# Kernel optimization log

Measured on AMD Instinct MI355X. Metric: run time of the kernel, lower is better.

The kernel has to match this reference:

```python
import jax, jax.numpy as jnp
import numpy as np

EPS = 1e-05
MARGIN = 0.0


def setup_inputs() -> dict:
    key = jax.random.key(0)
    k1, k2 = jax.random.split(key)
    embeddings = jax.random.normal(k1, (512, 512), dtype=jnp.float32)
    labels = jax.random.randint(k2, (512,), 0, 32, dtype=jnp.int64)
    return {"embeddings": embeddings, "labels": labels}


def _pairwise_distance(e, squared=False):
    # e: [B, D] -> [B, B] euclidean distances
    dot = jnp.matmul(e, e.T)
    sq = jnp.diag(dot)
    d = sq[:, None] - 2.0 * dot + sq[None, :]
    d = jnp.maximum(d, 0.0)
    if not squared:
        zmask = (d == 0.0).astype(d.dtype)
        d = d + zmask * EPS
        d = jnp.sqrt(d) + EPS
        d = d * (1.0 - zmask)
    return d


def _triplet_mask(labels):
    B = labels.shape[0]
    not_eq = ~jnp.eye(B, dtype=bool)
    # distinct indices i != j, i != k, j != k  -> [B, B, B]
    distinct = not_eq[:, :, None] & not_eq[:, None, :] & not_eq[None, :, :]
    lab_eq = labels[None, :] == labels[:, None]  # symmetric [B, B]
    valid = lab_eq[:, :, None] & (~lab_eq[:, None, :])  # label[i]==label[j], label[i]!=label[k]
    return (distinct & valid).astype(jnp.float32)


def reference(embeddings, labels):
    d = _pairwise_distance(embeddings, squared=False)  # [B, B]
    # triplet_loss[a, p, n] = d[a, p] - d[a, n] + margin
    tl = d[:, :, None] - d[:, None, :] + MARGIN
    mask = _triplet_mask(labels)
    tl = jnp.maximum(mask * tl, 0.0)
    num_positive = jnp.sum((tl > 1e-05).astype(jnp.float32))
    num_valid = jnp.sum(mask)
    fraction_positive = num_positive / (num_valid + 1e-05)
    loss = jnp.sum(tl) / (num_positive + 1e-05)
    return (loss, fraction_positive)
```

## Files before the change

### kernel.cpp

```cpp
#include <hip/hip_runtime.h>

#define BSZ 512
#define EPSF 1e-5f
#define KT   32
#define NS   16
#define TR   128
#define TC   64
#define ASTR 132
#define BSTR 68

#define WS_PARTIAL 8
#define WS_P       2048

__device__ __forceinline__ float dist_xform(float v) {
    v = fmaxf(v, 0.0f);
    float z = (v == 0.0f) ? 1.0f : 0.0f;
    v = sqrtf(v + z * EPSF) + EPSF;
    return v * (1.0f - z);
}

__global__ __launch_bounds__(256) void dsq_kernel(const float* __restrict__ E,
                                                  float* __restrict__ ws) {
    if (blockIdx.x == 0 && blockIdx.y == 0 && blockIdx.z == 0 && threadIdx.x == 0) {
        ((int*)ws)[3] = 0;
    }

    __shared__ __align__(16) float As[KT][ASTR];
    __shared__ __align__(16) float Bs[KT][BSTR];
    const int tid = threadIdx.x;
    const int tx = tid & 15;
    const int ty = tid >> 4;
    const int bi = blockIdx.x * TR;
    const int bj = blockIdx.y * TC;
    const int k0 = blockIdx.z * KT;

    {
        const int r0 = tid >> 3;
        const int kc = (tid & 7) * 4;
#pragma unroll
        for (int p = 0; p < 4; ++p) {
            const int row = p * 32 + r0;
            float4 v = *(const float4*)(E + (size_t)(bi + row) * BSZ + k0 + kc);
            As[kc  ][row] = v.x; As[kc+1][row] = v.y; As[kc+2][row] = v.z; As[kc+3][row] = v.w;
        }
#pragma unroll
        for (int p = 0; p < 2; ++p) {
            const int row = p * 32 + r0;
            float4 v = *(const float4*)(E + (size_t)(bj + row) * BSZ + k0 + kc);
            Bs[kc  ][row] = v.x; Bs[kc+1][row] = v.y; Bs[kc+2][row] = v.z; Bs[kc+3][row] = v.w;
        }
    }
    __syncthreads();

    float acc[8][4];
#pragma unroll
    for (int r = 0; r < 8; ++r)
#pragma unroll
        for (int c = 0; c < 4; ++c) acc[r][c] = 0.0f;

#pragma unroll 4
    for (int kk = 0; kk < KT; ++kk) {
        float4 A0 = *(const float4*)&As[kk][ty * 8];
        float4 A1 = *(const float4*)&As[kk][ty * 8 + 4];
        float4 B0 = *(const float4*)&Bs[kk][tx * 4];
        float ar[8] = {A0.x, A0.y, A0.z, A0.w, A1.x, A1.y, A1.z, A1.w};
        float br[4] = {B0.x, B0.y, B0.z, B0.w};
#pragma unroll
        for (int r = 0; r < 8; ++r)
#pragma unroll
            for (int c = 0; c < 4; ++c) {
                float d = ar[r] - br[c];
                acc[r][c] = fmaf(d, d, acc[r][c]);
            }
    }

    float* Pp = ws + WS_P + (size_t)blockIdx.z * BSZ * BSZ;
#pragma unroll
    for (int r = 0; r < 8; ++r) {
        float4 v = {acc[r][0], acc[r][1], acc[r][2], acc[r][3]};
        *(float4*)(Pp + (size_t)(bi + ty * 8 + r) * BSZ + bj + tx * 4) = v;
    }
}

__global__ __launch_bounds__(256) void triplet_kernel(const int* __restrict__ labels,
                                                      float* __restrict__ ws,
                                                      float* __restrict__ out) {
    const int a = blockIdx.x;
    const int tid = threadIdx.x;
    __shared__ float drow[BSZ];
    __shared__ int   lab[BSZ];
    __shared__ int   poslist[BSZ];
    __shared__ int   npos_s;
    __shared__ float wsum[4];
    __shared__ int   wcnt[4];
    __shared__ int   is_last;

    if (tid == 0) npos_s = 0;
    for (int t = tid; t < BSZ; t += 256) lab[t] = labels[t];

    const float* P = ws + WS_P;
    if (tid < 128) {
        float4 s4 = {0.f, 0.f, 0.f, 0.f};
#pragma unroll
        for (int s = 0; s < NS; ++s) {
            float4 v = *(const float4*)(P + ((size_t)s * BSZ + a) * BSZ + tid * 4);
            s4.x += v.x; s4.y += v.y; s4.z += v.z; s4.w += v.w;
        }
        drow[tid * 4 + 0] = dist_xform(s4.x);
        drow[tid * 4 + 1] = dist_xform(s4.y);
        drow[tid * 4 + 2] = dist_xform(s4.z);
        drow[tid * 4 + 3] = dist_xform(s4.w);
    }
    __syncthreads();

    const int la = lab[a];
    for (int t = tid; t < BSZ; t += 256) {
        if (lab[t] == la && t != a) {
            int idx = atomicAdd(&npos_s, 1);
            poslist[idx] = t;
        }
    }
    __syncthreads();

    const int npos = npos_s;
    const int nneg = BSZ - 1 - npos;
    float sum = 0.0f;
    int   cnt = 0;
    const int total = npos * BSZ;
    for (int idx = tid; idx < total; idx += 256) {
        const int p = poslist[idx >> 9];
        const int n = idx & (BSZ - 1);
        if (lab[n] != la) {
            const float v = drow[p] - drow[n];
            if (v > 0.0f)  sum += v;
            if (v > 1e-5f) cnt++;
        }
    }
#pragma unroll
    for (int off = 32; off > 0; off >>= 1) {
        sum += __shfl_down(sum, off);
        cnt += __shfl_down(cnt, off);
    }
    const int wave = tid >> 6, lane = tid & 63;
    if (lane == 0) { wsum[wave] = sum; wcnt[wave] = cnt; }
    __syncthreads();

    float* partial = ws + WS_PARTIAL;
    if (tid == 0) {
        partial[a]           = wsum[0] + wsum[1] + wsum[2] + wsum[3];
        partial[BSZ + a]     = (float)(wcnt[0] + wcnt[1] + wcnt[2] + wcnt[3]);
        partial[2*BSZ + a]   = (float)npos * (float)nneg;
        __threadfence();
        int old = atomicAdd((int*)ws + 3, 1);
        is_last = (old == BSZ - 1) ? 1 : 0;
    }
    __syncthreads();

    if (is_last) {
        __threadfence();
        float s = partial[tid]         + partial[tid + 256];
        float c = partial[BSZ + tid]   + partial[BSZ + tid + 256];
        float v = partial[2*BSZ + tid] + partial[2*BSZ + tid + 256];
#pragma unroll
        for (int off = 32; off > 0; off >>= 1) {
            s += __shfl_down(s, off);
            c += __shfl_down(c, off);
            v += __shfl_down(v, off);
        }
        if (lane == 0) { wsum[wave] = s; wcnt[wave] = (int)c; drow[wave] = v; }
        __syncthreads();
        if (tid == 0) {
            float S = wsum[0] + wsum[1] + wsum[2] + wsum[3];
            float C = (float)(wcnt[0] + wcnt[1] + wcnt[2] + wcnt[3]);
            float V = drow[0] + drow[1] + drow[2] + drow[3];
            out[0] = S / (C + 1e-5f);
            out[1] = C / (V + 1e-5f);
        }
    }
}

extern "C" void kernel_launch(void* const* d_in, const int* in_sizes, int n_in,
                              void* d_out, int out_size, void* d_ws, size_t ws_size,
                              hipStream_t stream) {
    const float* E      = (const float*)d_in[0];
    const int*   labels = (const int*)d_in[1];
    float* out = (float*)d_out;
    float* ws  = (float*)d_ws;

    dsq_kernel<<<dim3(4, 8, NS), 256, 0, stream>>>(E, ws);
    triplet_kernel<<<BSZ, 256, 0, stream>>>(labels, ws, out);
}
```

Measured before the change: 87.75 us.

## Fuse distance and triplet kernels into one launch with a grid-wide barrier

Merges the pairwise-distance partial kernel and the triplet reduction kernel into one kernel of 512 blocks. The two phases are separated by a software grid barrier: an atomic counter that each block spins on. A memset resets both counters before the launch. The intent is to remove the second kernel launch and the gap between launches, at the cost of a spin barrier that needs all 512 blocks resident at once. The launch bound of 4 blocks per SM is there to help make that possible, and deadlock is a risk if they are not all resident.

```diff
diff --git a/kernel.cpp b/kernel.cpp
--- a/kernel.cpp
+++ b/kernel.cpp
@@ -8,6 +8,7 @@
 #define TC   64
 #define ASTR 132
 #define BSTR 68
+#define NBLK 512
 
 #define WS_PARTIAL 8
 #define WS_P       2048
@@ -19,74 +20,15 @@
     return v * (1.0f - z);
 }
 
-__global__ __launch_bounds__(256) void dsq_kernel(const float* __restrict__ E,
-                                                  float* __restrict__ ws) {
-    if (blockIdx.x == 0 && blockIdx.y == 0 && blockIdx.z == 0 && threadIdx.x == 0) {
-        ((int*)ws)[3] = 0;
-    }
+__global__ __launch_bounds__(256, 4) void unified_kernel(const float* __restrict__ E,
+                                                         const int* __restrict__ labels,
+                                                         float* __restrict__ ws,
+                                                         float* __restrict__ out) {
+    const int tid = threadIdx.x;
+    const int b   = blockIdx.x;
 
     __shared__ __align__(16) float As[KT][ASTR];
     __shared__ __align__(16) float Bs[KT][BSTR];
-    const int tid = threadIdx.x;
-    const int tx = tid & 15;
-    const int ty = tid >> 4;
-    const int bi = blockIdx.x * TR;
-    const int bj = blockIdx.y * TC;
-    const int k0 = blockIdx.z * KT;
-
-    {
-        const int r0 = tid >> 3;
-        const int kc = (tid & 7) * 4;
-#pragma unroll
-        for (int p = 0; p < 4; ++p) {
-            const int row = p * 32 + r0;
-            float4 v = *(const float4*)(E + (size_t)(bi + row) * BSZ + k0 + kc);
-            As[kc  ][row] = v.x; As[kc+1][row] = v.y; As[kc+2][row] = v.z; As[kc+3][row] = v.w;
-        }
-#pragma unroll
-        for (int p = 0; p < 2; ++p) {
-            const int row = p * 32 + r0;
-            float4 v = *(const float4*)(E + (size_t)(bj + row) * BSZ + k0 + kc);
-            Bs[kc  ][row] = v.x; Bs[kc+1][row] = v.y; Bs[kc+2][row] = v.z; Bs[kc+3][row] = v.w;
-        }
-    }
-    __syncthreads();
-
-    float acc[8][4];
-#pragma unroll
-    for (int r = 0; r < 8; ++r)
-#pragma unroll
-        for (int c = 0; c < 4; ++c) acc[r][c] = 0.0f;
-
-#pragma unroll 4
-    for (int kk = 0; kk < KT; ++kk) {
-        float4 A0 = *(const float4*)&As[kk][ty * 8];
-        float4 A1 = *(const float4*)&As[kk][ty * 8 + 4];
-        float4 B0 = *(const float4*)&Bs[kk][tx * 4];
-        float ar[8] = {A0.x, A0.y, A0.z, A0.w, A1.x, A1.y, A1.z, A1.w};
-        float br[4] = {B0.x, B0.y, B0.z, B0.w};
-#pragma unroll
-        for (int r = 0; r < 8; ++r)
-#pragma unroll
-            for (int c = 0; c < 4; ++c) {
-                float d = ar[r] - br[c];
-                acc[r][c] = fmaf(d, d, acc[r][c]);
-            }
-    }
-
-    float* Pp = ws + WS_P + (size_t)blockIdx.z * BSZ * BSZ;
-#pragma unroll
-    for (int r = 0; r < 8; ++r) {
-        float4 v = {acc[r][0], acc[r][1], acc[r][2], acc[r][3]};
-        *(float4*)(Pp + (size_t)(bi + ty * 8 + r) * BSZ + bj + tx * 4) = v;
-    }
-}
-
-__global__ __launch_bounds__(256) void triplet_kernel(const int* __restrict__ labels,
-                                                      float* __restrict__ ws,
-                                                      float* __restrict__ out) {
-    const int a = blockIdx.x;
-    const int tid = threadIdx.x;
     __shared__ float drow[BSZ];
     __shared__ int   lab[BSZ];
     __shared__ int   poslist[BSZ];
@@ -95,6 +37,73 @@
     __shared__ int   wcnt[4];
     __shared__ int   is_last;
 
+    {
+        const int bi = (b & 3) * TR;
+        const int bj = ((b >> 2) & 7) * TC;
+        const int k0 = (b >> 5) * KT;
+
+        const int r0 = tid >> 3;
+        const int kc = (tid & 7) * 4;
+#pragma unroll
+        for (int p = 0; p < 4; ++p) {
+            const int row = p * 32 + r0;
+            float4 v = *(const float4*)(E + (size_t)(bi + row) * BSZ + k0 + kc);
+            As[kc  ][row] = v.x; As[kc+1][row] = v.y; As[kc+2][row] = v.z; As[kc+3][row] = v.w;
+        }
+#pragma unroll
+        for (int p = 0; p < 2; ++p) {
+            const int row = p * 32 + r0;
+            float4 v = *(const float4*)(E + (size_t)(bj + row) * BSZ + k0 + kc);
+            Bs[kc  ][row] = v.x; Bs[kc+1][row] = v.y; Bs[kc+2][row] = v.z; Bs[kc+3][row] = v.w;
+        }
+        __syncthreads();
+
+        const int tx = tid & 15;
+        const int ty = tid >> 4;
+        float acc[8][4];
+#pragma unroll
+        for (int r = 0; r < 8; ++r)
+#pragma unroll
+            for (int c = 0; c < 4; ++c) acc[r][c] = 0.0f;
+
+#pragma unroll 4
+        for (int kk = 0; kk < KT; ++kk) {
+            float4 A0 = *(const float4*)&As[kk][ty * 8];
+            float4 A1 = *(const float4*)&As[kk][ty * 8 + 4];
+            float4 B0 = *(const float4*)&Bs[kk][tx * 4];
+            float ar[8] = {A0.x, A0.y, A0.z, A0.w, A1.x, A1.y, A1.z, A1.w};
+            float br[4] = {B0.x, B0.y, B0.z, B0.w};
+#pragma unroll
+            for (int r = 0; r < 8; ++r)
+#pragma unroll
+                for (int c = 0; c < 4; ++c) {
+                    float d = ar[r] - br[c];
+                    acc[r][c] = fmaf(d, d, acc[r][c]);
+                }
+        }
+
+        float* Pp = ws + WS_P + (size_t)(b >> 5) * BSZ * BSZ;
+#pragma unroll
+        for (int r = 0; r < 8; ++r) {
+            float4 v = {acc[r][0], acc[r][1], acc[r][2], acc[r][3]};
+            *(float4*)(Pp + (size_t)(bi + ty * 8 + r) * BSZ + bj + tx * 4) = v;
+        }
+    }
+
+    __syncthreads();
+    unsigned int* cnt = (unsigned int*)ws;
+    if (tid == 0) {
+        __threadfence();
+        atomicAdd(&cnt[0], 1u);
+        while (__hip_atomic_load(&cnt[0], __ATOMIC_ACQUIRE,
+                                 __HIP_MEMORY_SCOPE_AGENT) < NBLK) {
+            __builtin_amdgcn_s_sleep(2);
+        }
+        __threadfence();
+    }
+    __syncthreads();
+
+    const int a = b;
     if (tid == 0) npos_s = 0;
     for (int t = tid; t < BSZ; t += 256) lab[t] = labels[t];
 
@@ -125,7 +134,7 @@
     const int npos = npos_s;
     const int nneg = BSZ - 1 - npos;
     float sum = 0.0f;
-    int   cnt = 0;
+    int   cnt2 = 0;
     const int total = npos * BSZ;
     for (int idx = tid; idx < total; idx += 256) {
         const int p = poslist[idx >> 9];
@@ -133,16 +142,16 @@
         if (lab[n] != la) {
             const float v = drow[p] - drow[n];
             if (v > 0.0f)  sum += v;
-            if (v > 1e-5f) cnt++;
+            if (v > 1e-5f) cnt2++;
         }
     }
 #pragma unroll
     for (int off = 32; off > 0; off >>= 1) {
-        sum += __shfl_down(sum, off);
-        cnt += __shfl_down(cnt, off);
+        sum  += __shfl_down(sum, off);
+        cnt2 += __shfl_down(cnt2, off);
     }
     const int wave = tid >> 6, lane = tid & 63;
-    if (lane == 0) { wsum[wave] = sum; wcnt[wave] = cnt; }
+    if (lane == 0) { wsum[wave] = sum; wcnt[wave] = cnt2; }
     __syncthreads();
 
     float* partial = ws + WS_PARTIAL;
@@ -151,8 +160,8 @@
         partial[BSZ + a]     = (float)(wcnt[0] + wcnt[1] + wcnt[2] + wcnt[3]);
         partial[2*BSZ + a]   = (float)npos * (float)nneg;
         __threadfence();
-        int old = atomicAdd((int*)ws + 3, 1);
-        is_last = (old == BSZ - 1) ? 1 : 0;
+        int old = atomicAdd((int*)&cnt[1], 1);
+        is_last = (old == NBLK - 1) ? 1 : 0;
     }
     __syncthreads();
 
@@ -187,6 +196,6 @@
     float* out = (float*)d_out;
     float* ws  = (float*)d_ws;
 
-    dsq_kernel<<<dim3(4, 8, NS), 256, 0, stream>>>(E, ws);
-    triplet_kernel<<<BSZ, 256, 0, stream>>>(labels, ws, out);
+    hipMemsetAsync(ws, 0, 8, stream);
+    unified_kernel<<<NBLK, 256, 0, stream>>>(E, labels, ws, out);
 }
```

Measured after the change: 148.6 us. 69.4% more time.

## Use square 64x64 distance tiles with halved K splits and separate final reduction kernel

Applied to the files above, without the earlier changes.

The pairwise squared-distance kernel moves to 64x64 output tiles with a K chunk of 64 and 8 K-splits instead of 16, which halves the partial-sum buffer the triplet kernel must read back and re-sum. The last-block atomic-counter reduction in the triplet kernel is replaced by a third single-block kernel that reduces the per-anchor partials. This drops the threadfence and atomic but adds one more kernel launch, and each thread now computes a smaller 4x4 register tile.

```diff
diff --git a/kernel.cpp b/kernel.cpp
--- a/kernel.cpp
+++ b/kernel.cpp
@@ -2,12 +2,10 @@
 
 #define BSZ 512
 #define EPSF 1e-5f
-#define KT   32
-#define NS   16
-#define TR   128
-#define TC   64
-#define ASTR 132
-#define BSTR 68
+#define KT   64
+#define NS   8
+#define TT   64
+#define LSTR 68
 
 #define WS_PARTIAL 8
 #define WS_P       2048
@@ -21,52 +19,43 @@
 
 __global__ __launch_bounds__(256) void dsq_kernel(const float* __restrict__ E,
                                                   float* __restrict__ ws) {
-    if (blockIdx.x == 0 && blockIdx.y == 0 && blockIdx.z == 0 && threadIdx.x == 0) {
-        ((int*)ws)[3] = 0;
-    }
-
-    __shared__ __align__(16) float As[KT][ASTR];
-    __shared__ __align__(16) float Bs[KT][BSTR];
+    __shared__ __align__(16) float As[KT][LSTR];
+    __shared__ __align__(16) float Bs[KT][LSTR];
     const int tid = threadIdx.x;
-    const int tx = tid & 15;
-    const int ty = tid >> 4;
-    const int bi = blockIdx.x * TR;
-    const int bj = blockIdx.y * TC;
+    const int bj = blockIdx.x * TT;
+    const int bi = blockIdx.y * TT;
     const int k0 = blockIdx.z * KT;
 
     {
-        const int r0 = tid >> 3;
-        const int kc = (tid & 7) * 4;
+        const int r0 = tid >> 4;
+        const int kc = (tid & 15) * 4;
 #pragma unroll
         for (int p = 0; p < 4; ++p) {
-            const int row = p * 32 + r0;
-            float4 v = *(const float4*)(E + (size_t)(bi + row) * BSZ + k0 + kc);
-            As[kc  ][row] = v.x; As[kc+1][row] = v.y; As[kc+2][row] = v.z; As[kc+3][row] = v.w;
-        }
-#pragma unroll
-        for (int p = 0; p < 2; ++p) {
-            const int row = p * 32 + r0;
-            float4 v = *(const float4*)(E + (size_t)(bj + row) * BSZ + k0 + kc);
-            Bs[kc  ][row] = v.x; Bs[kc+1][row] = v.y; Bs[kc+2][row] = v.z; Bs[kc+3][row] = v.w;
+            const int row = p * 16 + r0;
+            float4 va = *(const float4*)(E + (size_t)(bi + row) * BSZ + k0 + kc);
+            float4 vb = *(const float4*)(E + (size_t)(bj + row) * BSZ + k0 + kc);
+            As[kc  ][row] = va.x; As[kc+1][row] = va.y; As[kc+2][row] = va.z; As[kc+3][row] = va.w;
+            Bs[kc  ][row] = vb.x; Bs[kc+1][row] = vb.y; Bs[kc+2][row] = vb.z; Bs[kc+3][row] = vb.w;
         }
     }
     __syncthreads();
 
-    float acc[8][4];
+    const int tx = tid & 15;
+    const int ty = tid >> 4;
+    float acc[4][4];
 #pragma unroll
-    for (int r = 0; r < 8; ++r)
+    for (int r = 0; r < 4; ++r)
 #pragma unroll
         for (int c = 0; c < 4; ++c) acc[r][c] = 0.0f;
 
-#pragma unroll 4
+#pragma unroll 8
     for (int kk = 0; kk < KT; ++kk) {
-        float4 A0 = *(const float4*)&As[kk][ty * 8];
-        float4 A1 = *(const float4*)&As[kk][ty * 8 + 4];
+        float4 A0 = *(const float4*)&As[kk][ty * 4];
         float4 B0 = *(const float4*)&Bs[kk][tx * 4];
-        float ar[8] = {A0.x, A0.y, A0.z, A0.w, A1.x, A1.y, A1.z, A1.w};
+        float ar[4] = {A0.x, A0.y, A0.z, A0.w};
         float br[4] = {B0.x, B0.y, B0.z, B0.w};
 #pragma unroll
-        for (int r = 0; r < 8; ++r)
+        for (int r = 0; r < 4; ++r)
 #pragma unroll
             for (int c = 0; c < 4; ++c) {
                 float d = ar[r] - br[c];
@@ -76,15 +65,15 @@
 
     float* Pp = ws + WS_P + (size_t)blockIdx.z * BSZ * BSZ;
 #pragma unroll
-    for (int r = 0; r < 8; ++r) {
+    for (int r = 0; r < 4; ++r) {
         float4 v = {acc[r][0], acc[r][1], acc[r][2], acc[r][3]};
-        *(float4*)(Pp + (size_t)(bi + ty * 8 + r) * BSZ + bj + tx * 4) = v;
+        *(float4*)(Pp + (size_t)(bi + ty * 4 + r) * BSZ + bj + tx * 4) = v;
     }
 }
 
 __global__ __launch_bounds__(256) void triplet_kernel(const int* __restrict__ labels,
-                                                      float* __restrict__ ws,
-                                                      float* __restrict__ out) {
+                                                      const float* __restrict__ ws,
+                                                      float* __restrict__ partial) {
     const int a = blockIdx.x;
     const int tid = threadIdx.x;
     __shared__ float drow[BSZ];
@@ -93,23 +82,20 @@
     __shared__ int   npos_s;
     __shared__ float wsum[4];
     __shared__ int   wcnt[4];
-    __shared__ int   is_last;
 
     if (tid == 0) npos_s = 0;
     for (int t = tid; t < BSZ; t += 256) lab[t] = labels[t];
 
     const float* P = ws + WS_P;
-    if (tid < 128) {
-        float4 s4 = {0.f, 0.f, 0.f, 0.f};
+    {
+        float2 s2 = {0.f, 0.f};
 #pragma unroll
         for (int s = 0; s < NS; ++s) {
-            float4 v = *(const float4*)(P + ((size_t)s * BSZ + a) * BSZ + tid * 4);
-            s4.x += v.x; s4.y += v.y; s4.z += v.z; s4.w += v.w;
+            float2 v = *(const float2*)(P + ((size_t)s * BSZ + a) * BSZ + tid * 2);
+            s2.x += v.x; s2.y += v.y;
         }
-        drow[tid * 4 + 0] = dist_xform(s4.x);
-        drow[tid * 4 + 1] = dist_xform(s4.y);
-        drow[tid * 4 + 2] = dist_xform(s4.z);
-        drow[tid * 4 + 3] = dist_xform(s4.w);
+        drow[tid * 2 + 0] = dist_xform(s2.x);
+        drow[tid * 2 + 1] = dist_xform(s2.y);
     }
     __syncthreads();
 
@@ -144,38 +130,35 @@
     const int wave = tid >> 6, lane = tid & 63;
     if (lane == 0) { wsum[wave] = sum; wcnt[wave] = cnt; }
     __syncthreads();
-
-    float* partial = ws + WS_PARTIAL;
     if (tid == 0) {
         partial[a]           = wsum[0] + wsum[1] + wsum[2] + wsum[3];
         partial[BSZ + a]     = (float)(wcnt[0] + wcnt[1] + wcnt[2] + wcnt[3]);
         partial[2*BSZ + a]   = (float)npos * (float)nneg;
-        __threadfence();
-        int old = atomicAdd((int*)ws + 3, 1);
-        is_last = (old == BSZ - 1) ? 1 : 0;
     }
+}
+
+__global__ __launch_bounds__(256) void final_kernel(const float* __restrict__ partial,
+                                                    float* __restrict__ out) {
+    const int tid = threadIdx.x;
+    float s = partial[tid]         + partial[tid + 256];
+    float c = partial[BSZ + tid]   + partial[BSZ + tid + 256];
+    float v = partial[2*BSZ + tid] + partial[2*BSZ + tid + 256];
+#pragma unroll
+    for (int off = 32; off > 0; off >>= 1) {
+        s += __shfl_down(s, off);
+        c += __shfl_down(c, off);
+        v += __shfl_down(v, off);
+    }
+    __shared__ float ws_[4], wc[4], wv[4];
+    const int wave = tid >> 6, lane = tid & 63;
+    if (lane == 0) { ws_[wave] = s; wc[wave] = c; wv[wave] = v; }
     __syncthreads();
-
-    if (is_last) {
-        __threadfence();
-        float s = partial[tid]         + partial[tid + 256];
-        float c = partial[BSZ + tid]   + partial[BSZ + tid + 256];
-        float v = partial[2*BSZ + tid] + partial[2*BSZ + tid + 256];
-#pragma unroll
-        for (int off = 32; off > 0; off >>= 1) {
-            s += __shfl_down(s, off);
-            c += __shfl_down(c, off);
-            v += __shfl_down(v, off);
-        }
-        if (lane == 0) { wsum[wave] = s; wcnt[wave] = (int)c; drow[wave] = v; }
-        __syncthreads();
-        if (tid == 0) {
-            float S = wsum[0] + wsum[1] + wsum[2] + wsum[3];
-            float C = (float)(wcnt[0] + wcnt[1] + wcnt[2] + wcnt[3]);
-            float V = drow[0] + drow[1] + drow[2] + drow[3];
-            out[0] = S / (C + 1e-5f);
-            out[1] = C / (V + 1e-5f);
-        }
+    if (tid == 0) {
+        float S = ws_[0] + ws_[1] + ws_[2] + ws_[3];
+        float C = wc[0] + wc[1] + wc[2] + wc[3];
+        float V = wv[0] + wv[1] + wv[2] + wv[3];
+        out[0] = S / (C + 1e-5f);
+        out[1] = C / (V + 1e-5f);
     }
 }
 
@@ -186,7 +169,9 @@
     const int*   labels = (const int*)d_in[1];
     float* out = (float*)d_out;
     float* ws  = (float*)d_ws;
+    float* partial = ws + WS_PARTIAL;
 
-    dsq_kernel<<<dim3(4, 8, NS), 256, 0, stream>>>(E, ws);
-    triplet_kernel<<<BSZ, 256, 0, stream>>>(labels, ws, out);
+    dsq_kernel<<<dim3(8, 8, NS), 256, 0, stream>>>(E, ws);
+    triplet_kernel<<<BSZ, 256, 0, stream>>>(labels, ws, partial);
+    final_kernel<<<1, 256, 0, stream>>>(partial, out);
 }
```

New measurement: 79.73 us, median of 2. -9.1%, faster.

## Process two anchors per block and move final reduction to separate kernel

Applied to the files above, without the earlier changes.

Each triplet block now handles two anchor rows: it loads both distance rows at once using all 256 threads, then runs the per-anchor counting phase twice. The last-block-done atomic counter with thread fences is dropped, and a separate single-block kernel performs the final reduction instead. This halves the block count, uses every thread during the row load, and removes the atomic and fence handshake. In exchange it adds a third kernel launch and serialises two anchors inside each block.

```diff
diff --git a/kernel.cpp b/kernel.cpp
--- a/kernel.cpp
+++ b/kernel.cpp
@@ -1,6 +1,6 @@
 #include <hip/hip_runtime.h>
 
-#define BSZ 512
+#define BSZ  512
 #define EPSF 1e-5f
 #define KT   32
 #define NS   16
@@ -21,15 +21,9 @@
 
 __global__ __launch_bounds__(256) void dsq_kernel(const float* __restrict__ E,
                                                   float* __restrict__ ws) {
-    if (blockIdx.x == 0 && blockIdx.y == 0 && blockIdx.z == 0 && threadIdx.x == 0) {
-        ((int*)ws)[3] = 0;
-    }
-
     __shared__ __align__(16) float As[KT][ASTR];
     __shared__ __align__(16) float Bs[KT][BSTR];
     const int tid = threadIdx.x;
-    const int tx = tid & 15;
-    const int ty = tid >> 4;
     const int bi = blockIdx.x * TR;
     const int bj = blockIdx.y * TC;
     const int k0 = blockIdx.z * KT;
@@ -52,6 +46,8 @@
     }
     __syncthreads();
 
+    const int tx = tid & 15;
+    const int ty = tid >> 4;
     float acc[8][4];
 #pragma unroll
     for (int r = 0; r < 8; ++r)
@@ -82,48 +78,23 @@
     }
 }
 
-__global__ __launch_bounds__(256) void triplet_kernel(const int* __restrict__ labels,
-                                                      float* __restrict__ ws,
-                                                      float* __restrict__ out) {
-    const int a = blockIdx.x;
-    const int tid = threadIdx.x;
-    __shared__ float drow[BSZ];
-    __shared__ int   lab[BSZ];
-    __shared__ int   poslist[BSZ];
-    __shared__ int   npos_s;
-    __shared__ float wsum[4];
-    __shared__ int   wcnt[4];
-    __shared__ int   is_last;
-
-    if (tid == 0) npos_s = 0;
-    for (int t = tid; t < BSZ; t += 256) lab[t] = labels[t];
-
-    const float* P = ws + WS_P;
-    if (tid < 128) {
-        float4 s4 = {0.f, 0.f, 0.f, 0.f};
-#pragma unroll
-        for (int s = 0; s < NS; ++s) {
-            float4 v = *(const float4*)(P + ((size_t)s * BSZ + a) * BSZ + tid * 4);
-            s4.x += v.x; s4.y += v.y; s4.z += v.z; s4.w += v.w;
-        }
-        drow[tid * 4 + 0] = dist_xform(s4.x);
-        drow[tid * 4 + 1] = dist_xform(s4.y);
-        drow[tid * 4 + 2] = dist_xform(s4.z);
-        drow[tid * 4 + 3] = dist_xform(s4.w);
-    }
-    __syncthreads();
-
+__device__ __forceinline__ void triplet_phase(int a, const float* __restrict__ drow,
+                                              const int* lab, int* poslist,
+                                              int* npos_s, float* wsum, int* wcnt,
+                                              float* __restrict__ partial, int tid) {
+    if (tid == 0) *npos_s = 0;
+    __syncthreads();
     const int la = lab[a];
     for (int t = tid; t < BSZ; t += 256) {
         if (lab[t] == la && t != a) {
-            int idx = atomicAdd(&npos_s, 1);
+            int idx = atomicAdd(npos_s, 1);
             poslist[idx] = t;
         }
     }
     __syncthreads();
-
-    const int npos = npos_s;
+    const int npos = *npos_s;
     const int nneg = BSZ - 1 - npos;
+
     float sum = 0.0f;
     int   cnt = 0;
     const int total = npos * BSZ;
@@ -144,38 +115,73 @@
     const int wave = tid >> 6, lane = tid & 63;
     if (lane == 0) { wsum[wave] = sum; wcnt[wave] = cnt; }
     __syncthreads();
-
-    float* partial = ws + WS_PARTIAL;
     if (tid == 0) {
         partial[a]           = wsum[0] + wsum[1] + wsum[2] + wsum[3];
         partial[BSZ + a]     = (float)(wcnt[0] + wcnt[1] + wcnt[2] + wcnt[3]);
         partial[2*BSZ + a]   = (float)npos * (float)nneg;
-        __threadfence();
-        int old = atomicAdd((int*)ws + 3, 1);
-        is_last = (old == BSZ - 1) ? 1 : 0;
-    }
-    __syncthreads();
-
-    if (is_last) {
-        __threadfence();
-        float s = partial[tid]         + partial[tid + 256];
-        float c = partial[BSZ + tid]   + partial[BSZ + tid + 256];
-        float v = partial[2*BSZ + tid] + partial[2*BSZ + tid + 256];
-#pragma unroll
-        for (int off = 32; off > 0; off >>= 1) {
-            s += __shfl_down(s, off);
-            c += __shfl_down(c, off);
-            v += __shfl_down(v, off);
-        }
-        if (lane == 0) { wsum[wave] = s; wcnt[wave] = (int)c; drow[wave] = v; }
-        __syncthreads();
-        if (tid == 0) {
-            float S = wsum[0] + wsum[1] + wsum[2] + wsum[3];
-            float C = (float)(wcnt[0] + wcnt[1] + wcnt[2] + wcnt[3]);
-            float V = drow[0] + drow[1] + drow[2] + drow[3];
-            out[0] = S / (C + 1e-5f);
-            out[1] = C / (V + 1e-5f);
-        }
+    }
+    __syncthreads();
+}
+
+__global__ __launch_bounds__(256) void triplet_kernel(const int* __restrict__ labels,
+                                                      const float* __restrict__ ws,
+                                                      float* __restrict__ partial) {
+    const int a0 = blockIdx.x * 2;
+    const int tid = threadIdx.x;
+    __shared__ float drow[2][BSZ];
+    __shared__ int   lab[BSZ];
+    __shared__ int   poslist[BSZ];
+    __shared__ int   npos_s;
+    __shared__ float wsum[4];
+    __shared__ int   wcnt[4];
+
+    lab[tid]       = labels[tid];
+    lab[tid + 256] = labels[tid + 256];
+
+    const float* P = ws + WS_P;
+    {
+        const int half = tid >> 7;
+        const int q    = tid & 127;
+        const int a    = a0 + half;
+        float4 s4 = {0.f, 0.f, 0.f, 0.f};
+#pragma unroll
+        for (int s = 0; s < NS; ++s) {
+            float4 v = *(const float4*)(P + ((size_t)s * BSZ + a) * BSZ + q * 4);
+            s4.x += v.x; s4.y += v.y; s4.z += v.z; s4.w += v.w;
+        }
+        drow[half][q * 4 + 0] = dist_xform(s4.x);
+        drow[half][q * 4 + 1] = dist_xform(s4.y);
+        drow[half][q * 4 + 2] = dist_xform(s4.z);
+        drow[half][q * 4 + 3] = dist_xform(s4.w);
+    }
+    __syncthreads();
+
+    triplet_phase(a0,     drow[0], lab, poslist, &npos_s, wsum, wcnt, partial, tid);
+    triplet_phase(a0 + 1, drow[1], lab, poslist, &npos_s, wsum, wcnt, partial, tid);
+}
+
+__global__ __launch_bounds__(256) void final_kernel(const float* __restrict__ partial,
+                                                    float* __restrict__ out) {
+    const int tid = threadIdx.x;
+    float s = partial[tid]         + partial[tid + 256];
+    float c = partial[BSZ + tid]   + partial[BSZ + tid + 256];
+    float v = partial[2*BSZ + tid] + partial[2*BSZ + tid + 256];
+#pragma unroll
+    for (int off = 32; off > 0; off >>= 1) {
+        s += __shfl_down(s, off);
+        c += __shfl_down(c, off);
+        v += __shfl_down(v, off);
+    }
+    __shared__ float ws_[4], wc[4], wv[4];
+    const int wave = tid >> 6, lane = tid & 63;
+    if (lane == 0) { ws_[wave] = s; wc[wave] = c; wv[wave] = v; }
+    __syncthreads();
+    if (tid == 0) {
+        float S = ws_[0] + ws_[1] + ws_[2] + ws_[3];
+        float C = wc[0] + wc[1] + wc[2] + wc[3];
+        float V = wv[0] + wv[1] + wv[2] + wv[3];
+        out[0] = S / (C + 1e-5f);
+        out[1] = C / (V + 1e-5f);
     }
 }
 
@@ -186,7 +192,9 @@
     const int*   labels = (const int*)d_in[1];
     float* out = (float*)d_out;
     float* ws  = (float*)d_ws;
+    float* partial = ws + WS_PARTIAL;
 
     dsq_kernel<<<dim3(4, 8, NS), 256, 0, stream>>>(E, ws);
-    triplet_kernel<<<BSZ, 256, 0, stream>>>(labels, ws, out);
-}
+    triplet_kernel<<<BSZ / 2, 256, 0, stream>>>(labels, ws, partial);
+    final_kernel<<<1, 256, 0, stream>>>(partial, out);
+}
```

Measured after the change: 92.14 us. 1.05x slower.
